# Kernel optimization log

Measured on AMD Instinct MI355X. Metric: run time of the kernel, lower is better.

Reference implementation:

```python
import jax, jax.numpy as jnp
import numpy as np

S = 64    # shapelets_size
N = 256   # num_shapelets
C = 3     # in_channels
B = 64
L = 2048


def setup_inputs() -> dict:
    key = jax.random.key(0)
    kx, ks = jax.random.split(key)
    x = jax.random.normal(kx, (B, C, L), dtype=jnp.float32)
    shapelets = jax.random.normal(ks, (C, N, S), dtype=jnp.float32)
    return {"x": x, "shapelets": shapelets}


def reference(x, shapelets):
    # x: (B, C, L); shapelets: (C, N, S)
    W = x.shape[2] - S + 1  # number of sliding windows
    # unfold: (B, C, W, S)
    idx = jnp.arange(W)[:, None] + jnp.arange(S)[None, :]
    win = x[:, :, idx]
    # cdist with mm-based euclidean: d^2 = |a|^2 + |b|^2 - 2 a.b
    win_sq = jnp.sum(win * win, axis=-1)                 # (B, C, W)
    shp_sq = jnp.sum(shapelets * shapelets, axis=-1)     # (C, N)
    cross = jnp.einsum('bcws,cns->bcwn', win, shapelets)  # (B, C, W, N)
    d2 = win_sq[..., None] + shp_sq[None, :, None, :] - 2.0 * cross
    d = jnp.sqrt(jnp.maximum(d2, 0.0))                   # (B, C, W, N)
    # sum over channels, keepdim -> (B, 1, W, N); transpose -> (B, 1, N, W); min over W
    summed = jnp.sum(d, axis=1, keepdims=True)
    out = jnp.min(jnp.swapaxes(summed, 2, 3), axis=3)    # (B, 1, N)
    return out
```

## Files before the change

### kernel.cpp

```cpp
#include <hip/hip_runtime.h>
#include <hip/hip_fp16.h>


typedef float  v4f __attribute__((ext_vector_type(4)));
typedef unsigned int v4u __attribute__((ext_vector_type(4)));
typedef short  v8s __attribute__((ext_vector_type(8)));
typedef unsigned short u16;
typedef unsigned int   u32;
typedef unsigned long long u64;

#define N_ 256
#define C_ 3
#define L_ 2048
#define W_ 1985
#define XPAD 2176
#define CPY_U64 150
#define WL 512

#define OFF_GX   0u
#define OFF_HW   6684672u
#define OFF_SHP  7471104u
#define OFF_HS   7569408u

__device__ __forceinline__ u16 f2bf(float f) {
    u32 u = __builtin_bit_cast(u32, f);
    return (u16)((u + 0x7FFFu + ((u >> 16) & 1u)) >> 16);
}
__device__ __forceinline__ float bf2f(u16 b) {
    return __builtin_bit_cast(float, ((u32)b) << 16);
}
__device__ __forceinline__ u64 pack4(v4f v) {
    return (u64)f2bf(v[0]) | ((u64)f2bf(v[1]) << 16)
         | ((u64)f2bf(v[2]) << 32) | ((u64)f2bf(v[3]) << 48);
}

__global__ __launch_bounds__(256)
void prep_kernel(const float* __restrict__ x, const float* __restrict__ shp,
                 u16* __restrict__ gx, u16* __restrict__ ghw,
                 u16* __restrict__ gshp, float* __restrict__ ghs,
                 u32* __restrict__ out_u)
{
    const int blk = blockIdx.x, tid = threadIdx.x;
    if (blk < 192) {
        __shared__ u16 xb[2240];
        const int b = blk / 3, c = blk % 3;
        const float* xr = x + (size_t)(b * 3 + c) * L_;
        {
            v4f a0 = *(const v4f*)(xr + tid * 8);
            v4f a1 = *(const v4f*)(xr + tid * 8 + 4);
            ((u64*)xb)[tid * 2]     = pack4(a0);
            ((u64*)xb)[tid * 2 + 1] = pack4(a1);
            if (tid < 24) ((u64*)xb)[512 + tid] = 0;
        }
        __syncthreads();
        {
            const int r = tid >> 5, u0 = tid & 31;
            const bool odd = (r & 1);
            const int wadd = r >> 1;
            u16* grow = gx + ((size_t)(b * 3 + c) * 8 + r) * XPAD;
            const u32* lw = (const u32*)xb;
            #pragma unroll 1
            for (int i = 0; i < 9; ++i) {
                int u = u0 + i * 32;
                if (u < 272) {
                    u32 w[5];
                    #pragma unroll
                    for (int j = 0; j < 5; ++j) w[j] = lw[u * 4 + wadd + j];
                    v4u o;
                    #pragma unroll
                    for (int j = 0; j < 4; ++j) {
                        u32 sh = (w[j] >> 16) | (w[j + 1] << 16);
                        o[j] = odd ? sh : w[j];
                    }
                    *(v4u*)(grow + u * 8) = o;
                }
            }
        }
        {
            float e[80];
            #pragma unroll
            for (int j = 0; j < 20; ++j) {
                u64 ch = ((const u64*)xb)[tid * 2 + j];
                e[j * 4 + 0] = bf2f((u16)(ch));
                e[j * 4 + 1] = bf2f((u16)(ch >> 16));
                e[j * 4 + 2] = bf2f((u16)(ch >> 32));
                e[j * 4 + 3] = bf2f((u16)(ch >> 48));
            }
            float s = 0.f;
            #pragma unroll
            for (int i = 0; i < 64; ++i) s += e[i] * e[i];
            union { v4u v; __half h[8]; } hp;
            hp.h[0] = __float2half(-0.5f * s);
            #pragma unroll
            for (int k = 1; k < 8; ++k) {
                s += e[63 + k] * e[63 + k] - e[k - 1] * e[k - 1];
                hp.h[k] = __float2half(-0.5f * s);
            }
            *(v4u*)(ghw + (size_t)(b * 3 + c) * L_ + tid * 8) = hp.v;
        }
    } else if (blk < 195) {
        const int c = blk - 192;
        const int n = tid;
        const float* row = shp + ((size_t)c * N_ + n) * 64;
        float sacc = 0.f;
        #pragma unroll
        for (int k = 0; k < 8; ++k) {
            v4f a0 = *(const v4f*)(row + k * 8);
            v4f a1 = *(const v4f*)(row + k * 8 + 4);
            u64 p0 = pack4(a0), p1 = pack4(a1);
            union { u64 u[2]; v4u v; } st; st.u[0] = p0; st.u[1] = p1;
            *(v4u*)(gshp + ((size_t)c * N_ + n) * 64 + k * 8) = st.v;
            #pragma unroll
            for (int j = 0; j < 4; ++j) {
                float e0 = bf2f((u16)(p0 >> (16 * j)));
                float e1 = bf2f((u16)(p1 >> (16 * j)));
                sacc += e0 * e0 + e1 * e1;
            }
        }
        ghs[c * N_ + n] = -0.5f * sacc;
    } else {
        int i = (blk - 195) * 256 + tid;
        out_u[i] = 0x7F800000u;
    }
}

__global__ __launch_bounds__(256, 4)
void shapelet_min_kernel(const u16* __restrict__ gx, const u16* __restrict__ ghw,
                         const u16* __restrict__ gshp, const float* __restrict__ ghs,
                         u32* __restrict__ out_u)
{
    __shared__ __align__(16) u64 xcopy[C_ * 8 * CPY_U64];
    __shared__ __align__(16) __half hwq[C_ * WL];
    __shared__ float red[4][32];

    const int tid  = threadIdx.x;
    const int wave = tid >> 6;
    const int lane = tid & 63;
    const int m    = lane & 15;
    const int q    = lane >> 4;
    const int r    = m & 7;
    const int a    = m >> 3;
    const int wh   = blockIdx.x & 3;
    const int nb   = (blockIdx.x >> 2) & 7;
    const int b    = blockIdx.x >> 5;
    const int n0   = nb << 5;
    const int wstart = wh * WL;

    {
        const u16* gxb = gx + (size_t)b * 24 * XPAD;
        #pragma unroll
        for (int i = 0; i < 8; ++i) {
            int idx = tid + (i << 8);
            if (idx < 1800) {
                int cr = idx / 75;
                int u  = idx - cr * 75;
                v4u v = *(const v4u*)(gxb + cr * XPAD + wstart + u * 8);
                *(v4u*)((char*)xcopy + cr * 1200 + u * 16) = v;
            }
        }
    }
    if (tid < 192) {
        int c = tid >> 6, u = tid & 63;
        v4u v = *(const v4u*)(ghw + (size_t)(b * 3 + c) * L_ + wstart + u * 8);
        *(v4u*)((char*)hwq + c * 1024 + u * 16) = v;
    }
    v8s bfr[C_][2][2];
    float hs[C_][2];
    #pragma unroll
    for (int c = 0; c < C_; ++c)
        #pragma unroll
        for (int nt = 0; nt < 2; ++nt) {
            int n = n0 + nt * 16 + m;
            hs[c][nt] = ghs[c * N_ + n];
            #pragma unroll
            for (int h = 0; h < 2; ++h)
                bfr[c][nt][h] = *(const v8s*)(gshp + ((size_t)(c * N_ + n) * 64 + h * 32 + q * 8));
        }
    __syncthreads();

    float mins[2] = {1e30f, 1e30f};
    const int laneoff = q + a;

    #pragma unroll 1
    for (int it = 0; it < 4; ++it) {
        const int wb = it * 128 + wave * 32;
        if (wstart + wb >= W_) continue;

        float sums[2][2][4];
        #pragma unroll
        for (int mt = 0; mt < 2; ++mt)
            #pragma unroll
            for (int nt = 0; nt < 2; ++nt)
                #pragma unroll
                for (int g = 0; g < 4; ++g) sums[mt][nt][g] = 0.f;

        #pragma unroll
        for (int c = 0; c < C_; ++c) {
            v4f acc[2][2];
            #pragma unroll
            for (int mt = 0; mt < 2; ++mt) {
                union { u64 u; __half h4[4]; } wq;
                wq.u = *(const u64*)&hwq[c * WL + wb + mt * 16 + q * 4];
                #pragma unroll
                for (int g = 0; g < 4; ++g) {
                    float hv = __half2float(wq.h4[g]);
                    acc[mt][0][g] = hv + hs[c][0];
                    acc[mt][1][g] = hv + hs[c][1];
                }
            }
            const char* cb = (const char*)xcopy + (c * 8 + r) * 1200;
            #pragma unroll
            for (int h = 0; h < 2; ++h) {
                v8s afr[2];
                #pragma unroll
                for (int mt = 0; mt < 2; ++mt) {
                    int k = (wb >> 3) + mt * 2 + h * 4 + laneoff;
                    afr[mt] = *(const v8s*)(cb + k * 16);
                }
                #pragma unroll
                for (int mt = 0; mt < 2; ++mt)
                    #pragma unroll
                    for (int nt = 0; nt < 2; ++nt)
                        acc[mt][nt] = __builtin_amdgcn_mfma_f32_16x16x32_bf16(
                            afr[mt], bfr[c][nt][h], acc[mt][nt], 0, 0, 0);
            }
            #pragma unroll
            for (int mt = 0; mt < 2; ++mt)
                #pragma unroll
                for (int nt = 0; nt < 2; ++nt)
                    #pragma unroll
                    for (int g = 0; g < 4; ++g)
                        sums[mt][nt][g] += __builtin_amdgcn_sqrtf(fmaxf(-acc[mt][nt][g], 0.f));
        }
        #pragma unroll
        for (int mt = 0; mt < 2; ++mt) {
            #pragma unroll
            for (int g = 0; g < 4; ++g) {
                bool ok = (wstart + wb + mt * 16 + q * 4 + g) < W_;
                #pragma unroll
                for (int nt = 0; nt < 2; ++nt) {
                    float vv = ok ? sums[mt][nt][g] : 1e30f;
                    mins[nt] = fminf(mins[nt], vv);
                }
            }
        }
    }

    #pragma unroll
    for (int nt = 0; nt < 2; ++nt) {
        mins[nt] = fminf(mins[nt], __shfl_xor(mins[nt], 16));
        mins[nt] = fminf(mins[nt], __shfl_xor(mins[nt], 32));
    }
    if (lane < 16) { red[wave][m] = mins[0]; red[wave][16 + m] = mins[1]; }
    __syncthreads();
    if (tid < 32) {
        float v = fminf(fminf(red[0][tid], red[1][tid]),
                        fminf(red[2][tid], red[3][tid]));
        atomicMin(out_u + (size_t)b * N_ + n0 + tid,
                  __float_as_uint(v * 1.41421356237f));
    }
}

extern "C" void kernel_launch(void* const* d_in, const int* in_sizes, int n_in,
                              void* d_out, int out_size, void* d_ws, size_t ws_size,
                              hipStream_t stream) {
    const float* x   = (const float*)d_in[0];
    const float* shp = (const float*)d_in[1];
    u32* out_u       = (u32*)d_out;

    char* ws = (char*)d_ws;
    u16*   gx   = (u16*)(ws + OFF_GX);
    u16*   ghw  = (u16*)(ws + OFF_HW);
    u16*   gshp = (u16*)(ws + OFF_SHP);
    float* ghs  = (float*)(ws + OFF_HS);

    hipLaunchKernelGGL(prep_kernel, dim3(259), dim3(256), 0, stream,
                       x, shp, gx, ghw, gshp, ghs, out_u);
    hipLaunchKernelGGL(shapelet_min_kernel, dim3(2048), dim3(256), 0, stream,
                       gx, ghw, gshp, ghs, out_u);
}
```

Measured before the change: 104.0 us.

## Read bf16 windows directly from global memory with two shifted copies instead of LDS staging

The prep kernel now writes only two copies of each bf16 row (aligned and shifted by one element) instead of eight, and moves output initialisation into the x blocks. Out-of-range windows get a large negative half value so the main loop needs no bound checks. The main kernel drops its LDS staging and syncthreads, loading MFMA A fragments and window norms straight from global memory through cache. Each block now covers 1024 windows over 8 iterations, giving half as many blocks. This cuts prep write traffic and LDS setup, but depends on L1/L2 cache hits for unaligned global loads and lowers parallelism.

```diff
diff --git a/kernel.cpp b/kernel.cpp
--- a/kernel.cpp
+++ b/kernel.cpp
@@ -13,14 +13,12 @@
 #define C_ 3
 #define L_ 2048
 #define W_ 1985
-#define XPAD 2176
-#define CPY_U64 150
-#define WL 512
+#define XROW 2112
 
 #define OFF_GX   0u
-#define OFF_HW   6684672u
-#define OFF_SHP  7471104u
-#define OFF_HS   7569408u
+#define OFF_HW   1622016u
+#define OFF_SHP  2408448u
+#define OFF_HS   2506752u
 
 __device__ __forceinline__ u16 f2bf(float f) {
     u32 u = __builtin_bit_cast(u32, f);
@@ -42,44 +40,34 @@
 {
     const int blk = blockIdx.x, tid = threadIdx.x;
     if (blk < 192) {
-        __shared__ u16 xb[2240];
-        const int b = blk / 3, c = blk % 3;
-        const float* xr = x + (size_t)(b * 3 + c) * L_;
+        __shared__ u16 xb[2176];
+        const float* xr = x + (size_t)blk * L_;
+        v4f a0 = *(const v4f*)(xr + tid * 8);
+        v4f a1 = *(const v4f*)(xr + tid * 8 + 4);
+        ((u64*)xb)[tid * 2]     = pack4(a0);
+        ((u64*)xb)[tid * 2 + 1] = pack4(a1);
+        if (tid < 32) ((u64*)xb)[512 + tid] = 0;
+        if (blk < 64) out_u[blk * 256 + tid] = 0x7F800000u;
+        __syncthreads();
+
+        u16* g0 = gx + (size_t)blk * (2 * XROW);
+        const u32* lw = (const u32*)xb;
+        #pragma unroll 1
+        for (int u = tid; u < 264; u += 256) {
+            *(v4u*)(g0 + u * 8) = *(const v4u*)(xb + u * 8);
+            u32 w0 = lw[4 * u], w1 = lw[4 * u + 1], w2 = lw[4 * u + 2],
+                w3 = lw[4 * u + 3], w4 = lw[4 * u + 4];
+            v4u o;
+            o[0] = (w0 >> 16) | (w1 << 16);
+            o[1] = (w1 >> 16) | (w2 << 16);
+            o[2] = (w2 >> 16) | (w3 << 16);
+            o[3] = (w3 >> 16) | (w4 << 16);
+            *(v4u*)(g0 + XROW + u * 8) = o;
+        }
         {
-            v4f a0 = *(const v4f*)(xr + tid * 8);
-            v4f a1 = *(const v4f*)(xr + tid * 8 + 4);
-            ((u64*)xb)[tid * 2]     = pack4(a0);
-            ((u64*)xb)[tid * 2 + 1] = pack4(a1);
-            if (tid < 24) ((u64*)xb)[512 + tid] = 0;
-        }
-        __syncthreads();
-        {
-            const int r = tid >> 5, u0 = tid & 31;
-            const bool odd = (r & 1);
-            const int wadd = r >> 1;
-            u16* grow = gx + ((size_t)(b * 3 + c) * 8 + r) * XPAD;
-            const u32* lw = (const u32*)xb;
-            #pragma unroll 1
-            for (int i = 0; i < 9; ++i) {
-                int u = u0 + i * 32;
-                if (u < 272) {
-                    u32 w[5];
-                    #pragma unroll
-                    for (int j = 0; j < 5; ++j) w[j] = lw[u * 4 + wadd + j];
-                    v4u o;
-                    #pragma unroll
-                    for (int j = 0; j < 4; ++j) {
-                        u32 sh = (w[j] >> 16) | (w[j + 1] << 16);
-                        o[j] = odd ? sh : w[j];
-                    }
-                    *(v4u*)(grow + u * 8) = o;
-                }
-            }
-        }
-        {
-            float e[80];
-            #pragma unroll
-            for (int j = 0; j < 20; ++j) {
+            float e[72];
+            #pragma unroll
+            for (int j = 0; j < 18; ++j) {
                 u64 ch = ((const u64*)xb)[tid * 2 + j];
                 e[j * 4 + 0] = bf2f((u16)(ch));
                 e[j * 4 + 1] = bf2f((u16)(ch >> 16));
@@ -89,14 +77,15 @@
             float s = 0.f;
             #pragma unroll
             for (int i = 0; i < 64; ++i) s += e[i] * e[i];
+            const int w0 = tid * 8;
             union { v4u v; __half h[8]; } hp;
-            hp.h[0] = __float2half(-0.5f * s);
+            hp.h[0] = __float2half((w0 < W_) ? -0.5f * s : -65504.f);
             #pragma unroll
             for (int k = 1; k < 8; ++k) {
                 s += e[63 + k] * e[63 + k] - e[k - 1] * e[k - 1];
-                hp.h[k] = __float2half(-0.5f * s);
-            }
-            *(v4u*)(ghw + (size_t)(b * 3 + c) * L_ + tid * 8) = hp.v;
+                hp.h[k] = __float2half((w0 + k < W_) ? -0.5f * s : -65504.f);
+            }
+            *(v4u*)(ghw + (size_t)blk * L_ + w0) = hp.v;
         }
     } else if (blk < 195) {
         const int c = blk - 192;
@@ -118,9 +107,6 @@
             }
         }
         ghs[c * N_ + n] = -0.5f * sacc;
-    } else {
-        int i = (blk - 195) * 256 + tid;
-        out_u[i] = 0x7F800000u;
     }
 }
 
@@ -129,8 +115,6 @@
                          const u16* __restrict__ gshp, const float* __restrict__ ghs,
                          u32* __restrict__ out_u)
 {
-    __shared__ __align__(16) u64 xcopy[C_ * 8 * CPY_U64];
-    __shared__ __align__(16) __half hwq[C_ * WL];
     __shared__ float red[4][32];
 
     const int tid  = threadIdx.x;
@@ -138,33 +122,14 @@
     const int lane = tid & 63;
     const int m    = lane & 15;
     const int q    = lane >> 4;
-    const int r    = m & 7;
-    const int a    = m >> 3;
-    const int wh   = blockIdx.x & 3;
-    const int nb   = (blockIdx.x >> 2) & 7;
-    const int b    = blockIdx.x >> 5;
+    const int p    = m & 1;
+    const int wh   = blockIdx.x & 1;
+    const int nb   = (blockIdx.x >> 1) & 7;
+    const int b    = blockIdx.x >> 4;
     const int n0   = nb << 5;
-    const int wstart = wh * WL;
-
-    {
-        const u16* gxb = gx + (size_t)b * 24 * XPAD;
-        #pragma unroll
-        for (int i = 0; i < 8; ++i) {
-            int idx = tid + (i << 8);
-            if (idx < 1800) {
-                int cr = idx / 75;
-                int u  = idx - cr * 75;
-                v4u v = *(const v4u*)(gxb + cr * XPAD + wstart + u * 8);
-                *(v4u*)((char*)xcopy + cr * 1200 + u * 16) = v;
-            }
-        }
-    }
-    if (tid < 192) {
-        int c = tid >> 6, u = tid & 63;
-        v4u v = *(const v4u*)(ghw + (size_t)(b * 3 + c) * L_ + wstart + u * 8);
-        *(v4u*)((char*)hwq + c * 1024 + u * 16) = v;
-    }
-    v8s bfr[C_][2][2];
+    const int wstart = wh << 10;
+
+    v8s   bfr[C_][2][2];
     float hs[C_][2];
     #pragma unroll
     for (int c = 0; c < C_; ++c)
@@ -176,16 +141,20 @@
             for (int h = 0; h < 2; ++h)
                 bfr[c][nt][h] = *(const v8s*)(gshp + ((size_t)(c * N_ + n) * 64 + h * 32 + q * 8));
         }
-    __syncthreads();
+
+    const u16* pa[C_];
+    const u16* pw[C_];
+    #pragma unroll
+    for (int c = 0; c < C_; ++c) {
+        pa[c] = gx  + ((size_t)(b * 3 + c) * 2 + p) * XROW + (wstart + wave * 32 + m - p + q * 8);
+        pw[c] = ghw + (size_t)(b * 3 + c) * L_ + (wstart + wave * 32 + q * 4);
+    }
 
     float mins[2] = {1e30f, 1e30f};
-    const int laneoff = q + a;
 
     #pragma unroll 1
-    for (int it = 0; it < 4; ++it) {
-        const int wb = it * 128 + wave * 32;
-        if (wstart + wb >= W_) continue;
-
+    for (int it = 0; it < 8; ++it) {
+        const int iof = it * 128;
         float sums[2][2][4];
         #pragma unroll
         for (int mt = 0; mt < 2; ++mt)
@@ -200,7 +169,7 @@
             #pragma unroll
             for (int mt = 0; mt < 2; ++mt) {
                 union { u64 u; __half h4[4]; } wq;
-                wq.u = *(const u64*)&hwq[c * WL + wb + mt * 16 + q * 4];
+                __builtin_memcpy(&wq.u, pw[c] + iof + mt * 16, 8);
                 #pragma unroll
                 for (int g = 0; g < 4; ++g) {
                     float hv = __half2float(wq.h4[g]);
@@ -208,15 +177,12 @@
                     acc[mt][1][g] = hv + hs[c][1];
                 }
             }
-            const char* cb = (const char*)xcopy + (c * 8 + r) * 1200;
             #pragma unroll
             for (int h = 0; h < 2; ++h) {
                 v8s afr[2];
                 #pragma unroll
-                for (int mt = 0; mt < 2; ++mt) {
-                    int k = (wb >> 3) + mt * 2 + h * 4 + laneoff;
-                    afr[mt] = *(const v8s*)(cb + k * 16);
-                }
+                for (int mt = 0; mt < 2; ++mt)
+                    __builtin_memcpy(&afr[mt], pa[c] + iof + mt * 16 + h * 32, 16);
                 #pragma unroll
                 for (int mt = 0; mt < 2; ++mt)
                     #pragma unroll
@@ -233,17 +199,12 @@
                         sums[mt][nt][g] += __builtin_amdgcn_sqrtf(fmaxf(-acc[mt][nt][g], 0.f));
         }
         #pragma unroll
-        for (int mt = 0; mt < 2; ++mt) {
-            #pragma unroll
-            for (int g = 0; g < 4; ++g) {
-                bool ok = (wstart + wb + mt * 16 + q * 4 + g) < W_;
-                #pragma unroll
-                for (int nt = 0; nt < 2; ++nt) {
-                    float vv = ok ? sums[mt][nt][g] : 1e30f;
-                    mins[nt] = fminf(mins[nt], vv);
-                }
-            }
-        }
+        for (int mt = 0; mt < 2; ++mt)
+            #pragma unroll
+            for (int nt = 0; nt < 2; ++nt)
+                #pragma unroll
+                for (int g = 0; g < 4; ++g)
+                    mins[nt] = fminf(mins[nt], sums[mt][nt][g]);
     }
 
     #pragma unroll
@@ -274,8 +235,8 @@
     u16*   gshp = (u16*)(ws + OFF_SHP);
     float* ghs  = (float*)(ws + OFF_HS);
 
-    hipLaunchKernelGGL(prep_kernel, dim3(259), dim3(256), 0, stream,
+    hipLaunchKernelGGL(prep_kernel, dim3(195), dim3(256), 0, stream,
                        x, shp, gx, ghw, gshp, ghs, out_u);
-    hipLaunchKernelGGL(shapelet_min_kernel, dim3(2048), dim3(256), 0, stream,
+    hipLaunchKernelGGL(shapelet_min_kernel, dim3(1024), dim3(256), 0, stream,
                        gx, ghw, gshp, ghs, out_u);
 }
```

New measurement: 107.2 us. 1.03x slower.
